# Optimization experiments

Hardware: AMD Instinct MI355X
Metric: run time of the kernel (lower is better)

The kernel has to match this reference:

```python
import jax, jax.numpy as jnp
import numpy as np

D_MODEL = 256; N_HEADS = 8; HEAD_DIM = 32; N_LEVELS = 4; N_POINTS = 4; N_LAYERS = 3; D_FFN = 1024
SHAPES = np.array([[76, 76], [38, 38], [19, 19], [10, 10]], dtype=np.int64)
S_TOTAL = int((SHAPES[:, 0] * SHAPES[:, 1]).sum())  # 7681


def setup_inputs():
    key = jax.random.key(0)
    ks = jax.random.split(key, 12)
    B = 1; C = D_MODEL; M = N_HEADS; Lv = N_LEVELS; P = N_POINTS; L = N_LAYERS; s = 0.02
    starts = np.concatenate([[0], np.cumsum(SHAPES[:, 0] * SHAPES[:, 1])[:-1]]).astype(np.int64)
    inp = {
        "src": jax.random.normal(ks[0], (B, S_TOTAL, C), jnp.float32),
        "pos": jax.random.normal(ks[1], (B, S_TOTAL, C), jnp.float32),
        "valid_ratios": jnp.ones((B, Lv, 2), jnp.float32),
        "spatial_shapes": jnp.asarray(SHAPES),
        "level_start_index": jnp.asarray(starts),
        "padding_mask": jnp.zeros((B, S_TOTAL), bool),
        "W_off": jax.random.normal(ks[2], (L, C, M * Lv * P * 2), jnp.float32) * s,
        "b_off": jax.random.normal(ks[3], (L, M * Lv * P * 2), jnp.float32) * s,
        "W_attn": jax.random.normal(ks[4], (L, C, M * Lv * P), jnp.float32) * s,
        "b_attn": jax.random.normal(ks[5], (L, M * Lv * P), jnp.float32) * s,
        "W_val": jax.random.normal(ks[6], (L, C, C), jnp.float32) * s,
        "b_val": jnp.zeros((L, C), jnp.float32),
        "W_out": jax.random.normal(ks[7], (L, C, C), jnp.float32) * s,
        "b_out": jnp.zeros((L, C), jnp.float32),
        "ln1_g": jnp.ones((L, C), jnp.float32),
        "ln1_b": jnp.zeros((L, C), jnp.float32),
        "W_ff1": jax.random.normal(ks[8], (L, C, D_FFN), jnp.float32) * s,
        "b_ff1": jnp.zeros((L, D_FFN), jnp.float32),
        "W_ff2": jax.random.normal(ks[9], (L, D_FFN, C), jnp.float32) * s,
        "b_ff2": jnp.zeros((L, C), jnp.float32),
        "ln2_g": jnp.ones((L, C), jnp.float32),
        "ln2_b": jnp.zeros((L, C), jnp.float32),
    }
    return inp


def _ln(x, g, b):
    mu = x.mean(-1, keepdims=True)
    var = ((x - mu) ** 2).mean(-1, keepdims=True)
    return (x - mu) * jax.lax.rsqrt(var + 1e-5) * g + b


def _gather(v, idx):
    # v: [B, HW, M, D], idx: [B, S, M, P] -> [B, S, M, P, D], head-specific gather
    B, S, M, P = idx.shape
    def one(vb, ib):
        i2 = ib.transpose(0, 2, 1).reshape(S * P, M, 1)
        o = jnp.take_along_axis(vb, i2, axis=0)  # [S*P, M, D]
        return o.reshape(S, P, M, -1).transpose(0, 2, 1, 3)
    return jax.vmap(one)(v, idx)


def _msda(query, src, mask, ref, shapes, starts, Wo, bo, Wa, ba, Wv, bv, Wout, bout):
    # Multi-scale deformable attention (Deformable-DETR), grid_sample align_corners=False + zero padding
    B, S, C = src.shape
    M, Lv, P, D = N_HEADS, N_LEVELS, N_POINTS, HEAD_DIM
    value = src @ Wv + bv
    value = jnp.where(mask[..., None], 0.0, value).reshape(B, S, M, D)
    off = (query @ Wo + bo).reshape(B, S, M, Lv, P, 2)
    aw = jax.nn.softmax((query @ Wa + ba).reshape(B, S, M, Lv * P), -1).reshape(B, S, M, Lv, P)
    norm = jnp.asarray(shapes[:, ::-1].copy(), jnp.float32)  # (W, H) per level
    loc = ref[:, :, None, :, None, :] + off / norm[None, None, None, :, None, :]  # [B,S,M,Lv,P,2]
    out = jnp.zeros((B, S, M, D), query.dtype)
    for lvl in range(Lv):
        H = int(shapes[lvl, 0]); W = int(shapes[lvl, 1]); st = int(starts[lvl])
        v = value[:, st:st + H * W]  # [B, H*W, M, D]
        l = loc[:, :, :, lvl]  # [B, S, M, P, 2]
        x = l[..., 0] * W - 0.5
        y = l[..., 1] * H - 0.5
        x0 = jnp.floor(x); y0 = jnp.floor(y)
        dx = x - x0; dy = y - y0
        samp = jnp.zeros((B, S, M, P, D), query.dtype)
        for yy, xx, w in ((y0, x0, (1 - dy) * (1 - dx)), (y0, x0 + 1, (1 - dy) * dx),
                          (y0 + 1, x0, dy * (1 - dx)), (y0 + 1, x0 + 1, dy * dx)):
            valid = (xx >= 0) & (xx < W) & (yy >= 0) & (yy < H)
            xi = jnp.clip(xx, 0, W - 1).astype(jnp.int32)
            yi = jnp.clip(yy, 0, H - 1).astype(jnp.int32)
            g = _gather(v, yi * W + xi)
            samp = samp + (w * valid)[..., None] * g
        out = out + (aw[:, :, :, lvl, :, None] * samp).sum(3)
    return out.reshape(B, S, C) @ Wout + bout


def _ref_points(vr, shapes):
    refs = []
    for lvl in range(shapes.shape[0]):
        H = int(shapes[lvl, 0]); W = int(shapes[lvl, 1])
        ry, rx = np.meshgrid(np.linspace(0.5, H - 0.5, H, dtype=np.float32),
                             np.linspace(0.5, W - 0.5, W, dtype=np.float32), indexing="ij")
        rxj = jnp.asarray(rx.reshape(-1))[None] / (vr[:, None, lvl, 0] * W)
        ryj = jnp.asarray(ry.reshape(-1))[None] / (vr[:, None, lvl, 1] * H)
        refs.append(jnp.stack([rxj, ryj], -1))
    ref = jnp.concatenate(refs, 1)  # [B, S, 2]
    return ref[:, :, None] * vr[:, None]  # [B, S, Lv, 2]


def _encoder(src, pos, valid_ratios, shapes, starts, mask, params):
    (W_off, b_off, W_attn, b_attn, W_val, b_val, W_out, b_out,
     ln1_g, ln1_b, W_ff1, b_ff1, W_ff2, b_ff2, ln2_g, ln2_b) = params
    ref = _ref_points(valid_ratios, shapes)
    out = src
    for l in range(N_LAYERS):
        q = out + pos  # with_pos_embed
        a = _msda(q, out, mask, ref, shapes, starts, W_off[l], b_off[l], W_attn[l], b_attn[l],
                  W_val[l], b_val[l], W_out[l], b_out[l])
        out = _ln(out + a, ln1_g[l], ln1_b[l])
        f = jax.nn.relu(out @ W_ff1[l] + b_ff1[l]) @ W_ff2[l] + b_ff2[l]
        out = _ln(out + f, ln2_g[l], ln2_b[l])
    return out


def reference(src, pos, valid_ratios, spatial_shapes, level_start_index, padding_mask,
              W_off, b_off, W_attn, b_attn, W_val, b_val, W_out, b_out,
              ln1_g, ln1_b, W_ff1, b_ff1, W_ff2, b_ff2, ln2_g, ln2_b):
    shapes = np.asarray(spatial_shapes)
    starts = np.asarray(level_start_index)
    params = (W_off, b_off, W_attn, b_attn, W_val, b_val, W_out, b_out,
              ln1_g, ln1_b, W_ff1, b_ff1, W_ff2, b_ff2, ln2_g, ln2_b)
    return _encoder(src, pos, valid_ratios, shapes, starts, padding_mask, params)
```

## Files before the change

### kernel.cpp

```cpp
#include <hip/hip_runtime.h>
#include <hip/hip_bf16.h>
#include <math.h>

#define S_TOTAL 7681

typedef __attribute__((ext_vector_type(8))) short bf16x8;
typedef __attribute__((ext_vector_type(4))) float f32x4;

__device__ __forceinline__ short f2b(float x) {
    union { float f; unsigned u; } v; v.f = x;
    unsigned r = v.u + 0x7FFFu + ((v.u >> 16) & 1u);
    return (short)(r >> 16);
}
__device__ __forceinline__ float b2f(unsigned short u) {
    union { unsigned u; float f; } t; t.u = ((unsigned)u) << 16; return t.f;
}

__global__ __launch_bounds__(256) void transpose_cvt_kernel(
    const float* __restrict__ s0, const float* __restrict__ s1,
    const float* __restrict__ s2, const float* __restrict__ s3,
    const float* __restrict__ s4, const float* __restrict__ s5,
    short* __restrict__ d0, short* __restrict__ d1, short* __restrict__ d2,
    short* __restrict__ d3, short* __restrict__ d4, short* __restrict__ d5)
{
    const int z = blockIdx.z;
    int t = blockIdx.x;
    const float* src; short* dst; int K, N, lt;
    if (t < 64)       { src = s0 + (size_t)z * 65536;  dst = d0 + (size_t)z * 65536;  K = 256;  N = 256;  lt = t; }
    else if (t < 128) { src = s1 + (size_t)z * 65536;  dst = d1 + (size_t)z * 98304;  K = 256;  N = 256;  lt = t - 64; }
    else if (t < 160) { src = s2 + (size_t)z * 32768;  dst = d2 + (size_t)z * 98304;  K = 256;  N = 128;  lt = t - 128; }
    else if (t < 224) { src = s3 + (size_t)z * 65536;  dst = d3 + (size_t)z * 65536;  K = 256;  N = 256;  lt = t - 160; }
    else if (t < 480) { src = s4 + (size_t)z * 262144; dst = d4 + (size_t)z * 262144; K = 256;  N = 1024; lt = t - 224; }
    else              { src = s5 + (size_t)z * 262144; dst = d5 + (size_t)z * 262144; K = 1024; N = 256;  lt = t - 480; }
    const int ntx = N >> 5;
    const int tk = (lt / ntx) << 5, tn = (lt % ntx) << 5;
    __shared__ float tile[32][33];
    const int cx = threadIdx.x & 31, cy = threadIdx.x >> 5;
    #pragma unroll
    for (int i = 0; i < 32; i += 8)
        tile[cy + i][cx] = src[(size_t)(tk + cy + i) * N + tn + cx];
    __syncthreads();
    #pragma unroll
    for (int i = 0; i < 32; i += 8)
        dst[(size_t)(tn + cy + i) * K + tk + cx] = f2b(tile[cx][cy + i]);
}

#define BM 128
#define BN 64
#define BK 32
#define KP 40

__global__ __launch_bounds__(256) void gemm_va_kernel(
    const short* __restrict__ xb, const short* __restrict__ qb,
    const short* __restrict__ Wt_val, const short* __restrict__ Wt_oa,
    const float* __restrict__ b_val, const float* __restrict__ b_off,
    const float* __restrict__ b_attn,
    short* __restrict__ value_bf, float* __restrict__ offbuf, int M)
{
    const int grp = (blockIdx.y >= 4);
    const short* A  = grp ? qb : xb;
    const short* Wt = grp ? Wt_oa : Wt_val;
    const int colBase = (grp ? (blockIdx.y - 4) : blockIdx.y) * BN;
    const int N = grp ? 384 : 256;
    const int K = 256;

    __shared__ __align__(16) short As[BM * KP];
    __shared__ __align__(16) short Bs[BN * KP];
    const int tid = threadIdx.x;
    const int lane = tid & 63;
    const int wave = tid >> 6;
    const int rowBase = blockIdx.x * BM;

    const int ar = tid >> 1;
    const int ak = (tid & 1) * 16;
    const int br = tid >> 2;
    const int bk = (tid & 3) * 8;

    const int frow = lane & 15;
    const int fko  = (lane >> 4) * 8;
    const int wm = wave * 32;

    f32x4 acc[2][4] = {};

    const int aRow = rowBase + ar;
    const bool aOk = aRow < M;
    const short* Ap = A + (size_t)aRow * K + ak;
    const short* Bp = Wt + (size_t)(colBase + br) * K + bk;

    bf16x8 a0 = {}, a1 = {}, b0 = {};
    if (aOk) { a0 = *(const bf16x8*)Ap; a1 = *(const bf16x8*)(Ap + 8); }
    b0 = *(const bf16x8*)Bp;

    for (int k0 = 0; k0 < K; k0 += BK) {
        *(bf16x8*)&As[ar * KP + ak]     = a0;
        *(bf16x8*)&As[ar * KP + ak + 8] = a1;
        *(bf16x8*)&Bs[br * KP + bk]     = b0;
        __syncthreads();

        const int kn = k0 + BK;
        if (kn < K) {
            if (aOk) { a0 = *(const bf16x8*)(Ap + kn); a1 = *(const bf16x8*)(Ap + kn + 8); }
            b0 = *(const bf16x8*)(Bp + kn);
        }

        bf16x8 af0 = *(const bf16x8*)&As[(wm + frow) * KP + fko];
        bf16x8 af1 = *(const bf16x8*)&As[(wm + 16 + frow) * KP + fko];
        #pragma unroll
        for (int j = 0; j < 4; ++j) {
            bf16x8 bfj = *(const bf16x8*)&Bs[(j * 16 + frow) * KP + fko];
            acc[0][j] = __builtin_amdgcn_mfma_f32_16x16x32_bf16(af0, bfj, acc[0][j], 0, 0, 0);
            acc[1][j] = __builtin_amdgcn_mfma_f32_16x16x32_bf16(af1, bfj, acc[1][j], 0, 0, 0);
        }
        __syncthreads();
    }

    const int erow = (lane >> 4) * 4;
    const int ecol = lane & 15;
    #pragma unroll
    for (int mi = 0; mi < 2; ++mi) {
        #pragma unroll
        for (int j = 0; j < 4; ++j) {
            int col = colBase + j * 16 + ecol;
            float bias = grp ? (col < 256 ? b_off[col] : b_attn[col - 256]) : b_val[col];
            #pragma unroll
            for (int r = 0; r < 4; ++r) {
                int row = rowBase + wm + mi * 16 + erow + r;
                if (row < M) {
                    float v = acc[mi][j][r] + bias;
                    if (grp) offbuf[(size_t)row * 384 + col] = v;
                    else     value_bf[(size_t)row * 256 + col] = f2b(v);
                }
            }
        }
    }
}

template<int RELU, int OUTBF>
__global__ __launch_bounds__(256) void gemm_kernel(
    const short* __restrict__ A, const short* __restrict__ Wt,
    const float* __restrict__ bias, void* __restrict__ Cv,
    int M, int N, int K)
{
    __shared__ __align__(16) short As[BM * KP];
    __shared__ __align__(16) short Bs[BN * KP];
    const int tid = threadIdx.x;
    const int lane = tid & 63;
    const int wave = tid >> 6;
    const int rowBase = blockIdx.x * BM;
    const int colBase = blockIdx.y * BN;

    const int ar = tid >> 1;
    const int ak = (tid & 1) * 16;
    const int br = tid >> 2;
    const int bk = (tid & 3) * 8;

    const int frow = lane & 15;
    const int fko  = (lane >> 4) * 8;
    const int wm = wave * 32;

    f32x4 acc[2][4] = {};

    const int aRow = rowBase + ar;
    const bool aOk = aRow < M;
    const short* Ap = A + (size_t)aRow * K + ak;
    const short* Bp = Wt + (size_t)(colBase + br) * K + bk;

    bf16x8 a0 = {}, a1 = {}, b0 = {};
    if (aOk) { a0 = *(const bf16x8*)Ap; a1 = *(const bf16x8*)(Ap + 8); }
    b0 = *(const bf16x8*)Bp;

    for (int k0 = 0; k0 < K; k0 += BK) {
        *(bf16x8*)&As[ar * KP + ak]     = a0;
        *(bf16x8*)&As[ar * KP + ak + 8] = a1;
        *(bf16x8*)&Bs[br * KP + bk]     = b0;
        __syncthreads();

        const int kn = k0 + BK;
        if (kn < K) {
            if (aOk) { a0 = *(const bf16x8*)(Ap + kn); a1 = *(const bf16x8*)(Ap + kn + 8); }
            b0 = *(const bf16x8*)(Bp + kn);
        }

        bf16x8 af0 = *(const bf16x8*)&As[(wm + frow) * KP + fko];
        bf16x8 af1 = *(const bf16x8*)&As[(wm + 16 + frow) * KP + fko];
        #pragma unroll
        for (int j = 0; j < 4; ++j) {
            bf16x8 bfj = *(const bf16x8*)&Bs[(j * 16 + frow) * KP + fko];
            acc[0][j] = __builtin_amdgcn_mfma_f32_16x16x32_bf16(af0, bfj, acc[0][j], 0, 0, 0);
            acc[1][j] = __builtin_amdgcn_mfma_f32_16x16x32_bf16(af1, bfj, acc[1][j], 0, 0, 0);
        }
        __syncthreads();
    }

    const int erow = (lane >> 4) * 4;
    const int ecol = lane & 15;
    #pragma unroll
    for (int mi = 0; mi < 2; ++mi) {
        #pragma unroll
        for (int j = 0; j < 4; ++j) {
            #pragma unroll
            for (int r = 0; r < 4; ++r) {
                int row = rowBase + wm + mi * 16 + erow + r;
                if (row < M) {
                    int col = colBase + j * 16 + ecol;
                    float v = acc[mi][j][r] + bias[col];
                    if (RELU) v = fmaxf(v, 0.f);
                    if (OUTBF) ((short*)Cv)[(size_t)row * N + col] = f2b(v);
                    else       ((float*)Cv)[(size_t)row * N + col] = v;
                }
            }
        }
    }
}

template<int WRITEQ>
__global__ __launch_bounds__(256) void gemm_ln_kernel(
    const short* __restrict__ A, const short* __restrict__ Wt,
    const float* __restrict__ bias, const float* __restrict__ g,
    const float* __restrict__ bln, const float* __restrict__ pos,
    float* __restrict__ out, short* __restrict__ xb, short* __restrict__ qb,
    int M, int K)
{
    __shared__ __align__(16) short As[32 * KP];
    __shared__ __align__(16) short Bs[256 * KP];
    __shared__ float rsum[32][4], rsq[32][4], smu[32], srs[32];

    const int tid = threadIdx.x;
    const int lane = tid & 63;
    const int wave = tid >> 6;
    const int rowBase = blockIdx.x * 32;

    const int frow = lane & 15;
    const int fko  = (lane >> 4) * 8;

    f32x4 acc[2][4] = {};

    const int ar = tid >> 1;
    const int ak = (tid & 1) * 16;
    const int aRow = rowBase + ar;
    const bool aOk = (tid < 64) && (aRow < M);
    const short* Ap = A + (size_t)aRow * K + ak;
    const short* Bp = Wt + (size_t)tid * K;

    bf16x8 a0 = {}, a1 = {};
    bf16x8 w0, w1, w2, w3;
    if (aOk) { a0 = *(const bf16x8*)Ap; a1 = *(const bf16x8*)(Ap + 8); }
    w0 = *(const bf16x8*)(Bp);      w1 = *(const bf16x8*)(Bp + 8);
    w2 = *(const bf16x8*)(Bp + 16); w3 = *(const bf16x8*)(Bp + 24);

    for (int k0 = 0; k0 < K; k0 += BK) {
        if (tid < 64) {
            *(bf16x8*)&As[ar * KP + ak]     = a0;
            *(bf16x8*)&As[ar * KP + ak + 8] = a1;
        }
        *(bf16x8*)&Bs[tid * KP + 0]  = w0;
        *(bf16x8*)&Bs[tid * KP + 8]  = w1;
        *(bf16x8*)&Bs[tid * KP + 16] = w2;
        *(bf16x8*)&Bs[tid * KP + 24] = w3;
        __syncthreads();

        const int kn = k0 + BK;
        if (kn < K) {
            if (aOk) { a0 = *(const bf16x8*)(Ap + kn); a1 = *(const bf16x8*)(Ap + kn + 8); }
            w0 = *(const bf16x8*)(Bp + kn);      w1 = *(const bf16x8*)(Bp + kn + 8);
            w2 = *(const bf16x8*)(Bp + kn + 16); w3 = *(const bf16x8*)(Bp + kn + 24);
        }

        bf16x8 af0 = *(const bf16x8*)&As[frow * KP + fko];
        bf16x8 af1 = *(const bf16x8*)&As[(16 + frow) * KP + fko];
        #pragma unroll
        for (int j = 0; j < 4; ++j) {
            bf16x8 bfj = *(const bf16x8*)&Bs[(wave * 64 + j * 16 + frow) * KP + fko];
            acc[0][j] = __builtin_amdgcn_mfma_f32_16x16x32_bf16(af0, bfj, acc[0][j], 0, 0, 0);
            acc[1][j] = __builtin_amdgcn_mfma_f32_16x16x32_bf16(af1, bfj, acc[1][j], 0, 0, 0);
        }
        __syncthreads();
    }

    const int erow = (lane >> 4) * 4;
    const int ecol = lane & 15;
    float x[2][4][4];
    #pragma unroll
    for (int mi = 0; mi < 2; ++mi)
        #pragma unroll
        for (int j = 0; j < 4; ++j)
            #pragma unroll
            for (int r = 0; r < 4; ++r) {
                int row = rowBase + mi * 16 + erow + r;
                int col = wave * 64 + j * 16 + ecol;
                float res = (row < M) ? out[(size_t)row * 256 + col] : 0.f;
                x[mi][j][r] = acc[mi][j][r] + bias[col] + res;
            }

    #pragma unroll
    for (int mi = 0; mi < 2; ++mi)
        #pragma unroll
        for (int r = 0; r < 4; ++r) {
            float s1 = x[mi][0][r] + x[mi][1][r] + x[mi][2][r] + x[mi][3][r];
            float s2 = x[mi][0][r]*x[mi][0][r] + x[mi][1][r]*x[mi][1][r]
                     + x[mi][2][r]*x[mi][2][r] + x[mi][3][r]*x[mi][3][r];
            #pragma unroll
            for (int o = 1; o < 16; o <<= 1) {
                s1 += __shfl_xor(s1, o);
                s2 += __shfl_xor(s2, o);
            }
            if ((lane & 15) == 0) {
                rsum[mi * 16 + erow + r][wave] = s1;
                rsq [mi * 16 + erow + r][wave] = s2;
            }
        }
    __syncthreads();
    if (tid < 32) {
        float S1 = rsum[tid][0] + rsum[tid][1] + rsum[tid][2] + rsum[tid][3];
        float S2 = rsq[tid][0] + rsq[tid][1] + rsq[tid][2] + rsq[tid][3];
        float mu = S1 * (1.f / 256.f);
        smu[tid] = mu;
        srs[tid] = rsqrtf(S2 * (1.f / 256.f) - mu * mu + 1e-5f);
    }
    __syncthreads();

    #pragma unroll
    for (int mi = 0; mi < 2; ++mi)
        #pragma unroll
        for (int r = 0; r < 4; ++r) {
            int lrow = mi * 16 + erow + r;
            int row = rowBase + lrow;
            if (row >= M) continue;
            float mu = smu[lrow], rs = srs[lrow];
            #pragma unroll
            for (int j = 0; j < 4; ++j) {
                int col = wave * 64 + j * 16 + ecol;
                float y = (x[mi][j][r] - mu) * rs * g[col] + bln[col];
                out[(size_t)row * 256 + col] = y;
                xb[(size_t)row * 256 + col] = f2b(y);
                if (WRITEQ)
                    qb[(size_t)row * 256 + col] = f2b(y + pos[(size_t)row * 256 + col]);
            }
        }
}

__global__ __launch_bounds__(256) void msda_kernel(
    const short* __restrict__ value, const float* __restrict__ offb,
    short* __restrict__ msdab)
{
    __shared__ float   soff[8 * 384];
    __shared__ ushort4 sIdx[1024];
    __shared__ float4  sWgt[1024];

    const int bid = blockIdx.x;
    const int sb = (bid & 7) * 121 + (bid >> 3);
    const int q0 = sb * 8;
    if (q0 >= S_TOTAL) return;
    const int tid = threadIdx.x;

    {
        const float4* src4 = (const float4*)offb;
        #pragma unroll
        for (int i = tid; i < 768; i += 256) {
            int qi = i / 96, j = i - qi * 96;
            int q = min(q0 + qi, S_TOTAL - 1);
            *(float4*)&soff[qi * 384 + j * 4] = src4[(size_t)q * 96 + j];
        }
    }
    __syncthreads();

    if (tid < 64) {
        const int qi = tid >> 3, m = tid & 7;
        float* lg = &soff[qi * 384 + 256 + m * 16];
        float mx = -1e30f;
        #pragma unroll
        for (int k = 0; k < 16; ++k) mx = fmaxf(mx, lg[k]);
        float e[16], sum = 0.f;
        #pragma unroll
        for (int k = 0; k < 16; ++k) { e[k] = expf(lg[k] - mx); sum += e[k]; }
        float inv = 1.f / sum;
        #pragma unroll
        for (int k = 0; k < 16; ++k) lg[k] = e[k] * inv;
    }
    __syncthreads();

    #pragma unroll
    for (int it = tid; it < 1024; it += 256) {
        const int qi = it >> 7, i = it & 127;
        const int lvl = (i >> 2) & 3;
        const int q = min(q0 + qi, S_TOTAL - 1);

        float refx, refy;
        if (q < 5776)      { int t = q;        int r = t / 76, c = t % 76; refx = (c + 0.5f) / 76.f; refy = (r + 0.5f) / 76.f; }
        else if (q < 7220) { int t = q - 5776; int r = t / 38, c = t % 38; refx = (c + 0.5f) / 38.f; refy = (r + 0.5f) / 38.f; }
        else if (q < 7581) { int t = q - 7220; int r = t / 19, c = t % 19; refx = (c + 0.5f) / 19.f; refy = (r + 0.5f) / 19.f; }
        else               { int t = q - 7581; int r = t / 10, c = t % 10; refx = (c + 0.5f) / 10.f; refy = (r + 0.5f) / 10.f; }

        const int LVL_HW[4] = {76, 38, 19, 10};
        const int LVL_ST[4] = {0, 5776, 7220, 7581};
        const int W = LVL_HW[lvl];
        const float fW = (float)W;

        float ox = soff[qi * 384 + i * 2];
        float oy = soff[qi * 384 + i * 2 + 1];
        float aw = soff[qi * 384 + 256 + i];

        float x = refx * fW + ox - 0.5f;
        float y = refy * fW + oy - 0.5f;
        float x0f = floorf(x), y0f = floorf(y);
        int x0 = (int)x0f, y0 = (int)y0f;
        float dx = x - x0f, dy = y - y0f;

        bool vx0 = (x0 >= 0) & (x0 < W);
        bool vx1 = (x0 >= -1) & (x0 < W - 1);
        bool vy0 = (y0 >= 0) & (y0 < W);
        bool vy1 = (y0 >= -1) & (y0 < W - 1);
        int xc0 = min(max(x0, 0), W - 1), xc1 = min(max(x0 + 1, 0), W - 1);
        int yc0 = min(max(y0, 0), W - 1), yc1 = min(max(y0 + 1, 0), W - 1);
        int base = LVL_ST[lvl];
        ushort4 id;
        id.x = (unsigned short)(base + yc0 * W + xc0);
        id.y = (unsigned short)(base + yc0 * W + xc1);
        id.z = (unsigned short)(base + yc1 * W + xc0);
        id.w = (unsigned short)(base + yc1 * W + xc1);
        float4 w4;
        w4.x = (vy0 && vx0) ? (1.f - dy) * (1.f - dx) * aw : 0.f;
        w4.y = (vy0 && vx1) ? (1.f - dy) * dx * aw : 0.f;
        w4.z = (vy1 && vx0) ? dy * (1.f - dx) * aw : 0.f;
        w4.w = (vy1 && vx1) ? dy * dx * aw : 0.f;
        sIdx[it] = id;
        sWgt[it] = w4;
    }
    __syncthreads();

    const int lane = tid & 63;
    const int qi = (tid >> 6) * 2 + (lane >> 5);
    const int q = q0 + qi;
    if (q >= S_TOTAL) return;
    const int l32 = lane & 31;
    const int h = l32 >> 2, dg = l32 & 3;
    const short* vcol = value + h * 32 + dg * 8;
    const int itb = qi * 128 + (h << 4);

    float a[8] = {};
    #pragma unroll
    for (int pt = 0; pt < 16; ++pt) {
        const ushort4 id = sIdx[itb + pt];
        const float4 w = sWgt[itb + pt];
        bf16x8 v0 = *(const bf16x8*)(vcol + ((size_t)id.x << 8));
        bf16x8 v1 = *(const bf16x8*)(vcol + ((size_t)id.y << 8));
        bf16x8 v2 = *(const bf16x8*)(vcol + ((size_t)id.z << 8));
        bf16x8 v3 = *(const bf16x8*)(vcol + ((size_t)id.w << 8));
        #pragma unroll
        for (int e = 0; e < 8; ++e)
            a[e] += w.x * b2f((unsigned short)v0[e]) + w.y * b2f((unsigned short)v1[e])
                  + w.z * b2f((unsigned short)v2[e]) + w.w * b2f((unsigned short)v3[e]);
    }
    bf16x8 o;
    #pragma unroll
    for (int e = 0; e < 8; ++e) o[e] = f2b(a[e]);
    *(bf16x8*)(msdab + (size_t)q * 256 + h * 32 + dg * 8) = o;
}

__global__ __launch_bounds__(256) void cvt_copy_kernel(
    const float4* __restrict__ src, const float4* __restrict__ pos,
    float4* __restrict__ o, ushort4* __restrict__ xb, ushort4* __restrict__ qb,
    int n4)
{
    int i = blockIdx.x * blockDim.x + threadIdx.x;
    if (i < n4) {
        float4 v = src[i], p = pos[i];
        o[i] = v;
        ushort4 h, hq;
        h.x = (unsigned short)f2b(v.x); h.y = (unsigned short)f2b(v.y);
        h.z = (unsigned short)f2b(v.z); h.w = (unsigned short)f2b(v.w);
        hq.x = (unsigned short)f2b(v.x + p.x); hq.y = (unsigned short)f2b(v.y + p.y);
        hq.z = (unsigned short)f2b(v.z + p.z); hq.w = (unsigned short)f2b(v.w + p.w);
        xb[i] = h;
        qb[i] = hq;
    }
}

extern "C" void kernel_launch(void* const* d_in, const int* in_sizes, int n_in,
                              void* d_out, int out_size, void* d_ws, size_t ws_size,
                              hipStream_t stream) {
    const float* src    = (const float*)d_in[0];
    const float* pos    = (const float*)d_in[1];
    const float* W_off  = (const float*)d_in[6];
    const float* b_off  = (const float*)d_in[7];
    const float* W_attn = (const float*)d_in[8];
    const float* b_attn = (const float*)d_in[9];
    const float* W_val  = (const float*)d_in[10];
    const float* b_val  = (const float*)d_in[11];
    const float* W_out  = (const float*)d_in[12];
    const float* b_out  = (const float*)d_in[13];
    const float* ln1_g  = (const float*)d_in[14];
    const float* ln1_b  = (const float*)d_in[15];
    const float* W_ff1  = (const float*)d_in[16];
    const float* b_ff1  = (const float*)d_in[17];
    const float* W_ff2  = (const float*)d_in[18];
    const float* b_ff2  = (const float*)d_in[19];
    const float* ln2_g  = (const float*)d_in[20];
    const float* ln2_b  = (const float*)d_in[21];

    const size_t S = S_TOTAL;
    float* out = (float*)d_out;

    short* wt = (short*)d_ws;
    short* Wt_val = wt;
    short* Wt_oa  = wt + 196608;
    short* Wt_out = wt + 491520;
    short* Wt_ff1 = wt + 688128;
    short* Wt_ff2 = wt + 1474560;
    float* fbase  = (float*)d_ws + 1131648;
    short* xb       = (short*)fbase;
    short* qb       = (short*)(fbase + 128 * S);
    short* value_bf = (short*)(fbase + 256 * S);
    float* offb     = fbase + 384 * S;
    short* msdab    = (short*)(fbase + 768 * S);
    short* hid      = (short*)(fbase + 256 * S);

    transpose_cvt_kernel<<<dim3(736, 1, 3), 256, 0, stream>>>(
        W_val, W_off, W_attn, W_out, W_ff1, W_ff2,
        Wt_val, Wt_oa, Wt_oa + 65536, Wt_out, Wt_ff1, Wt_ff2);

    const int n4 = (int)(S * 256 / 4);
    const int g4 = (n4 + 255) / 256;
    cvt_copy_kernel<<<g4, 256, 0, stream>>>((const float4*)src, (const float4*)pos,
                                            (float4*)out, (ushort4*)xb, (ushort4*)qb, n4);

    const int MB = (S_TOTAL + BM - 1) / BM;
    const int LB = (S_TOTAL + 31) / 32;

    for (int l = 0; l < 3; ++l) {
        gemm_va_kernel<<<dim3(MB, 10), 256, 0, stream>>>(
            xb, qb, Wt_val + (size_t)l * 65536, Wt_oa + (size_t)l * 98304,
            b_val + (size_t)l * 256, b_off + (size_t)l * 256, b_attn + (size_t)l * 128,
            value_bf, offb, S_TOTAL);
        msda_kernel<<<968, 256, 0, stream>>>(value_bf, offb, msdab);
        gemm_ln_kernel<0><<<LB, 256, 0, stream>>>(
            msdab, Wt_out + (size_t)l * 65536, b_out + (size_t)l * 256,
            ln1_g + (size_t)l * 256, ln1_b + (size_t)l * 256, pos,
            out, xb, qb, S_TOTAL, 256);
        gemm_kernel<1, 1><<<dim3(MB, 16), 256, 0, stream>>>(
            xb, Wt_ff1 + (size_t)l * 262144, b_ff1 + (size_t)l * 1024, hid,
            S_TOTAL, 1024, 256);
        gemm_ln_kernel<1><<<LB, 256, 0, stream>>>(
            hid, Wt_ff2 + (size_t)l * 262144, b_ff2 + (size_t)l * 256,
            ln2_g + (size_t)l * 256, ln2_b + (size_t)l * 256, pos,
            out, xb, qb, S_TOTAL, 1024);
    }
}
```

Baseline: 415.8 us.

## Fuse MSDA sampling into out-projection+LayerNorm and merge prologue kernels

The deformable-attention sampling kernel is fused with the output projection GEMM and LayerNorm. Each 16-row block samples its queries into shared memory and feeds them straight to MFMA, so the intermediate msda buffer no longer round-trips through global memory. The FF2+LN kernel now uses 16-row tiles, giving more blocks, and the weight transpose and input convert kernels are merged into one launch. In exchange, every 16-row block reloads the full out-projection and FF2 weights, and the fused kernel uses more shared memory, which may lower occupancy.

```diff
diff --git a/kernel.cpp b/kernel.cpp
--- a/kernel.cpp
+++ b/kernel.cpp
@@ -16,39 +16,58 @@
     union { unsigned u; float f; } t; t.u = ((unsigned)u) << 16; return t.f;
 }
 
-__global__ __launch_bounds__(256) void transpose_cvt_kernel(
+#define BM 128
+#define BN 64
+#define BK 32
+#define KP 40
+
+#define N4_TOT 491584
+__global__ __launch_bounds__(256) void prologue_kernel(
     const float* __restrict__ s0, const float* __restrict__ s1,
     const float* __restrict__ s2, const float* __restrict__ s3,
     const float* __restrict__ s4, const float* __restrict__ s5,
     short* __restrict__ d0, short* __restrict__ d1, short* __restrict__ d2,
-    short* __restrict__ d3, short* __restrict__ d4, short* __restrict__ d5)
+    short* __restrict__ d3, short* __restrict__ d4, short* __restrict__ d5,
+    const float4* __restrict__ src, const float4* __restrict__ pos,
+    float4* __restrict__ o, ushort4* __restrict__ xb, ushort4* __restrict__ qb)
 {
-    const int z = blockIdx.z;
-    int t = blockIdx.x;
-    const float* src; short* dst; int K, N, lt;
-    if (t < 64)       { src = s0 + (size_t)z * 65536;  dst = d0 + (size_t)z * 65536;  K = 256;  N = 256;  lt = t; }
-    else if (t < 128) { src = s1 + (size_t)z * 65536;  dst = d1 + (size_t)z * 98304;  K = 256;  N = 256;  lt = t - 64; }
-    else if (t < 160) { src = s2 + (size_t)z * 32768;  dst = d2 + (size_t)z * 98304;  K = 256;  N = 128;  lt = t - 128; }
-    else if (t < 224) { src = s3 + (size_t)z * 65536;  dst = d3 + (size_t)z * 65536;  K = 256;  N = 256;  lt = t - 160; }
-    else if (t < 480) { src = s4 + (size_t)z * 262144; dst = d4 + (size_t)z * 262144; K = 256;  N = 1024; lt = t - 224; }
-    else              { src = s5 + (size_t)z * 262144; dst = d5 + (size_t)z * 262144; K = 1024; N = 256;  lt = t - 480; }
+    int b = blockIdx.x;
+    if (b >= 2208) {
+        int i = (b - 2208) * 256 + threadIdx.x;
+        if (i < N4_TOT) {
+            float4 v = src[i], p = pos[i];
+            o[i] = v;
+            ushort4 h, hq;
+            h.x = (unsigned short)f2b(v.x); h.y = (unsigned short)f2b(v.y);
+            h.z = (unsigned short)f2b(v.z); h.w = (unsigned short)f2b(v.w);
+            hq.x = (unsigned short)f2b(v.x + p.x); hq.y = (unsigned short)f2b(v.y + p.y);
+            hq.z = (unsigned short)f2b(v.z + p.z); hq.w = (unsigned short)f2b(v.w + p.w);
+            xb[i] = h;
+            qb[i] = hq;
+        }
+        return;
+    }
+    const int z = b / 736;
+    int t = b - z * 736;
+    const float* src_w; short* dst; int K, N, lt;
+    if (t < 64)       { src_w = s0 + (size_t)z * 65536;  dst = d0 + (size_t)z * 65536;  K = 256;  N = 256;  lt = t; }
+    else if (t < 128) { src_w = s1 + (size_t)z * 65536;  dst = d1 + (size_t)z * 98304;  K = 256;  N = 256;  lt = t - 64; }
+    else if (t < 160) { src_w = s2 + (size_t)z * 32768;  dst = d2 + (size_t)z * 98304;  K = 256;  N = 128;  lt = t - 128; }
+    else if (t < 224) { src_w = s3 + (size_t)z * 65536;  dst = d3 + (size_t)z * 65536;  K = 256;  N = 256;  lt = t - 160; }
+    else if (t < 480) { src_w = s4 + (size_t)z * 262144; dst = d4 + (size_t)z * 262144; K = 256;  N = 1024; lt = t - 224; }
+    else              { src_w = s5 + (size_t)z * 262144; dst = d5 + (size_t)z * 262144; K = 1024; N = 256;  lt = t - 480; }
     const int ntx = N >> 5;
     const int tk = (lt / ntx) << 5, tn = (lt % ntx) << 5;
     __shared__ float tile[32][33];
     const int cx = threadIdx.x & 31, cy = threadIdx.x >> 5;
     #pragma unroll
     for (int i = 0; i < 32; i += 8)
-        tile[cy + i][cx] = src[(size_t)(tk + cy + i) * N + tn + cx];
+        tile[cy + i][cx] = src_w[(size_t)(tk + cy + i) * N + tn + cx];
     __syncthreads();
     #pragma unroll
     for (int i = 0; i < 32; i += 8)
         dst[(size_t)(tn + cy + i) * K + tk + cx] = f2b(tile[cx][cy + i]);
 }
-
-#define BM 128
-#define BN 64
-#define BK 32
-#define KP 40
 
 __global__ __launch_bounds__(256) void gemm_va_kernel(
     const short* __restrict__ xb, const short* __restrict__ qb,
@@ -61,7 +80,6 @@
     const short* A  = grp ? qb : xb;
     const short* Wt = grp ? Wt_oa : Wt_val;
     const int colBase = (grp ? (blockIdx.y - 4) : blockIdx.y) * BN;
-    const int N = grp ? 384 : 256;
     const int K = 256;
 
     __shared__ __align__(16) short As[BM * KP];
@@ -135,10 +153,9 @@
     }
 }
 
-template<int RELU, int OUTBF>
-__global__ __launch_bounds__(256) void gemm_kernel(
+__global__ __launch_bounds__(256) void gemm_ff1_kernel(
     const short* __restrict__ A, const short* __restrict__ Wt,
-    const float* __restrict__ bias, void* __restrict__ Cv,
+    const float* __restrict__ bias, short* __restrict__ Cv,
     int M, int N, int K)
 {
     __shared__ __align__(16) short As[BM * KP];
@@ -203,53 +220,261 @@
                 int row = rowBase + wm + mi * 16 + erow + r;
                 if (row < M) {
                     int col = colBase + j * 16 + ecol;
-                    float v = acc[mi][j][r] + bias[col];
-                    if (RELU) v = fmaxf(v, 0.f);
-                    if (OUTBF) ((short*)Cv)[(size_t)row * N + col] = f2b(v);
-                    else       ((float*)Cv)[(size_t)row * N + col] = v;
+                    float v = fmaxf(acc[mi][j][r] + bias[col], 0.f);
+                    Cv[(size_t)row * N + col] = f2b(v);
                 }
             }
         }
     }
 }
 
+__global__ __launch_bounds__(256) void msda_outln_kernel(
+    const short* __restrict__ value, const float* __restrict__ offb,
+    const short* __restrict__ Wt_out, const float* __restrict__ bias,
+    const float* __restrict__ g, const float* __restrict__ bln,
+    float* __restrict__ out, short* __restrict__ xb, int M)
+{
+    __shared__ __align__(16) char scratch[36864];
+    __shared__ __align__(16) short mt[16 * 264];
+    __shared__ float rsum[16][4], rsq[16][4], smu[16], srs[16];
+    float*   soff = (float*)scratch;
+    ushort4* sIdx = (ushort4*)(scratch + 12288);
+    float4*  sWgt = (float4*)(scratch + 20480);
+    short*   Bs   = (short*)scratch;
+
+    const int bid = blockIdx.x;
+    const int sb = (bid < 480) ? ((bid & 7) * 60 + (bid >> 3)) : 480;
+    const int q0 = sb * 16;
+    const int tid = threadIdx.x;
+    const int lane = tid & 63;
+    const int wave = tid >> 6;
+
+    for (int t = 0; t < 2; ++t) {
+        const int qs = q0 + t * 8;
+        {
+            const float4* src4 = (const float4*)offb;
+            float4* soff4 = (float4*)soff;
+            #pragma unroll
+            for (int i = tid; i < 768; i += 256) {
+                int qi = i / 96, j = i - qi * 96;
+                int q = min(qs + qi, S_TOTAL - 1);
+                soff4[qi * 96 + j] = src4[(size_t)q * 96 + j];
+            }
+        }
+        __syncthreads();
+
+        if (tid < 64) {
+            const int qi = tid >> 3, m = tid & 7;
+            float* lg = &soff[qi * 384 + 256 + m * 16];
+            float mx = -1e30f;
+            #pragma unroll
+            for (int k = 0; k < 16; ++k) mx = fmaxf(mx, lg[k]);
+            float e[16], sum = 0.f;
+            #pragma unroll
+            for (int k = 0; k < 16; ++k) { e[k] = expf(lg[k] - mx); sum += e[k]; }
+            float inv = 1.f / sum;
+            #pragma unroll
+            for (int k = 0; k < 16; ++k) lg[k] = e[k] * inv;
+        }
+        __syncthreads();
+
+        #pragma unroll
+        for (int it = tid; it < 1024; it += 256) {
+            const int qi = it >> 7, i = it & 127;
+            const int lvl = (i >> 2) & 3;
+            const int q = min(qs + qi, S_TOTAL - 1);
+
+            float refx, refy;
+            if (q < 5776)      { int u = q;        int r = u / 76, c = u % 76; refx = (c + 0.5f) / 76.f; refy = (r + 0.5f) / 76.f; }
+            else if (q < 7220) { int u = q - 5776; int r = u / 38, c = u % 38; refx = (c + 0.5f) / 38.f; refy = (r + 0.5f) / 38.f; }
+            else if (q < 7581) { int u = q - 7220; int r = u / 19, c = u % 19; refx = (c + 0.5f) / 19.f; refy = (r + 0.5f) / 19.f; }
+            else               { int u = q - 7581; int r = u / 10, c = u % 10; refx = (c + 0.5f) / 10.f; refy = (r + 0.5f) / 10.f; }
+
+            const int LVL_HW[4] = {76, 38, 19, 10};
+            const int LVL_ST[4] = {0, 5776, 7220, 7581};
+            const int W = LVL_HW[lvl];
+            const float fW = (float)W;
+
+            float ox = soff[qi * 384 + i * 2];
+            float oy = soff[qi * 384 + i * 2 + 1];
+            float aw = soff[qi * 384 + 256 + i];
+
+            float x = refx * fW + ox - 0.5f;
+            float y = refy * fW + oy - 0.5f;
+            float x0f = floorf(x), y0f = floorf(y);
+            int x0 = (int)x0f, y0 = (int)y0f;
+            float dx = x - x0f, dy = y - y0f;
+
+            bool vx0 = (x0 >= 0) & (x0 < W);
+            bool vx1 = (x0 >= -1) & (x0 < W - 1);
+            bool vy0 = (y0 >= 0) & (y0 < W);
+            bool vy1 = (y0 >= -1) & (y0 < W - 1);
+            int xc0 = min(max(x0, 0), W - 1), xc1 = min(max(x0 + 1, 0), W - 1);
+            int yc0 = min(max(y0, 0), W - 1), yc1 = min(max(y0 + 1, 0), W - 1);
+            int base = LVL_ST[lvl];
+            ushort4 id;
+            id.x = (unsigned short)(base + yc0 * W + xc0);
+            id.y = (unsigned short)(base + yc0 * W + xc1);
+            id.z = (unsigned short)(base + yc1 * W + xc0);
+            id.w = (unsigned short)(base + yc1 * W + xc1);
+            float4 w4;
+            w4.x = (vy0 && vx0) ? (1.f - dy) * (1.f - dx) * aw : 0.f;
+            w4.y = (vy0 && vx1) ? (1.f - dy) * dx * aw : 0.f;
+            w4.z = (vy1 && vx0) ? dy * (1.f - dx) * aw : 0.f;
+            w4.w = (vy1 && vx1) ? dy * dx * aw : 0.f;
+            sIdx[it] = id;
+            sWgt[it] = w4;
+        }
+        __syncthreads();
+
+        {
+            const int qi = wave * 2 + ((lane >> 5) & 1);
+            const int l32 = lane & 31;
+            const int h = l32 >> 2, dg = l32 & 3;
+            const short* vcol = value + h * 32 + dg * 8;
+            const int itb = qi * 128 + (h << 4);
+
+            float a[8] = {};
+            #pragma unroll
+            for (int pt = 0; pt < 16; ++pt) {
+                const ushort4 id = sIdx[itb + pt];
+                const float4 w = sWgt[itb + pt];
+                bf16x8 v0 = *(const bf16x8*)(vcol + ((size_t)id.x << 8));
+                bf16x8 v1 = *(const bf16x8*)(vcol + ((size_t)id.y << 8));
+                bf16x8 v2 = *(const bf16x8*)(vcol + ((size_t)id.z << 8));
+                bf16x8 v3 = *(const bf16x8*)(vcol + ((size_t)id.w << 8));
+                #pragma unroll
+                for (int e = 0; e < 8; ++e)
+                    a[e] += w.x * b2f((unsigned short)v0[e]) + w.y * b2f((unsigned short)v1[e])
+                          + w.z * b2f((unsigned short)v2[e]) + w.w * b2f((unsigned short)v3[e]);
+            }
+            bf16x8 o;
+            #pragma unroll
+            for (int e = 0; e < 8; ++e) o[e] = f2b(a[e]);
+            *(bf16x8*)&mt[(t * 8 + qi) * 264 + h * 32 + dg * 8] = o;
+        }
+        __syncthreads();
+    }
+
+    const int frow = lane & 15;
+    const int fko  = (lane >> 4) * 8;
+
+    f32x4 acc[4] = {};
+    const short* Bp = Wt_out + (size_t)tid * 256;
+    bf16x8 w0 = *(const bf16x8*)(Bp);      bf16x8 w1 = *(const bf16x8*)(Bp + 8);
+    bf16x8 w2 = *(const bf16x8*)(Bp + 16); bf16x8 w3 = *(const bf16x8*)(Bp + 24);
+
+    for (int k0 = 0; k0 < 256; k0 += BK) {
+        *(bf16x8*)&Bs[tid * KP + 0]  = w0;
+        *(bf16x8*)&Bs[tid * KP + 8]  = w1;
+        *(bf16x8*)&Bs[tid * KP + 16] = w2;
+        *(bf16x8*)&Bs[tid * KP + 24] = w3;
+        __syncthreads();
+
+        const int kn = k0 + BK;
+        if (kn < 256) {
+            w0 = *(const bf16x8*)(Bp + kn);      w1 = *(const bf16x8*)(Bp + kn + 8);
+            w2 = *(const bf16x8*)(Bp + kn + 16); w3 = *(const bf16x8*)(Bp + kn + 24);
+        }
+
+        bf16x8 af = *(const bf16x8*)&mt[frow * 264 + k0 + fko];
+        #pragma unroll
+        for (int j = 0; j < 4; ++j) {
+            bf16x8 bfj = *(const bf16x8*)&Bs[(wave * 64 + j * 16 + frow) * KP + fko];
+            acc[j] = __builtin_amdgcn_mfma_f32_16x16x32_bf16(af, bfj, acc[j], 0, 0, 0);
+        }
+        __syncthreads();
+    }
+
+    const int erow = (lane >> 4) * 4;
+    const int ecol = lane & 15;
+    float x[4][4];
+    #pragma unroll
+    for (int j = 0; j < 4; ++j)
+        #pragma unroll
+        for (int r = 0; r < 4; ++r) {
+            int row = q0 + erow + r;
+            int col = wave * 64 + j * 16 + ecol;
+            float res = (row < M) ? out[(size_t)row * 256 + col] : 0.f;
+            x[j][r] = acc[j][r] + bias[col] + res;
+        }
+
+    #pragma unroll
+    for (int r = 0; r < 4; ++r) {
+        float s1 = x[0][r] + x[1][r] + x[2][r] + x[3][r];
+        float s2 = x[0][r]*x[0][r] + x[1][r]*x[1][r] + x[2][r]*x[2][r] + x[3][r]*x[3][r];
+        #pragma unroll
+        for (int o = 1; o < 16; o <<= 1) {
+            s1 += __shfl_xor(s1, o);
+            s2 += __shfl_xor(s2, o);
+        }
+        if ((lane & 15) == 0) {
+            rsum[erow + r][wave] = s1;
+            rsq [erow + r][wave] = s2;
+        }
+    }
+    __syncthreads();
+    if (tid < 16) {
+        float S1 = rsum[tid][0] + rsum[tid][1] + rsum[tid][2] + rsum[tid][3];
+        float S2 = rsq[tid][0] + rsq[tid][1] + rsq[tid][2] + rsq[tid][3];
+        float mu = S1 * (1.f / 256.f);
+        smu[tid] = mu;
+        srs[tid] = rsqrtf(S2 * (1.f / 256.f) - mu * mu + 1e-5f);
+    }
+    __syncthreads();
+
+    #pragma unroll
+    for (int r = 0; r < 4; ++r) {
+        int lrow = erow + r;
+        int row = q0 + lrow;
+        if (row >= M) continue;
+        float mu = smu[lrow], rs = srs[lrow];
+        #pragma unroll
+        for (int j = 0; j < 4; ++j) {
+            int col = wave * 64 + j * 16 + ecol;
+            float y = (x[j][r] - mu) * rs * g[col] + bln[col];
+            out[(size_t)row * 256 + col] = y;
+            xb[(size_t)row * 256 + col] = f2b(y);
+        }
+    }
+}
+
 template<int WRITEQ>
-__global__ __launch_bounds__(256) void gemm_ln_kernel(
+__global__ __launch_bounds__(256) void gemm_ln16_kernel(
     const short* __restrict__ A, const short* __restrict__ Wt,
     const float* __restrict__ bias, const float* __restrict__ g,
     const float* __restrict__ bln, const float* __restrict__ pos,
     float* __restrict__ out, short* __restrict__ xb, short* __restrict__ qb,
     int M, int K)
 {
-    __shared__ __align__(16) short As[32 * KP];
+    __shared__ __align__(16) short As[16 * KP];
     __shared__ __align__(16) short Bs[256 * KP];
-    __shared__ float rsum[32][4], rsq[32][4], smu[32], srs[32];
+    __shared__ float rsum[16][4], rsq[16][4], smu[16], srs[16];
 
     const int tid = threadIdx.x;
     const int lane = tid & 63;
     const int wave = tid >> 6;
-    const int rowBase = blockIdx.x * 32;
+    const int rowBase = blockIdx.x * 16;
 
     const int frow = lane & 15;
     const int fko  = (lane >> 4) * 8;
 
-    f32x4 acc[2][4] = {};
+    f32x4 acc[4] = {};
 
     const int ar = tid >> 1;
     const int ak = (tid & 1) * 16;
     const int aRow = rowBase + ar;
-    const bool aOk = (tid < 64) && (aRow < M);
+    const bool aOk = (tid < 32) && (aRow < M);
     const short* Ap = A + (size_t)aRow * K + ak;
     const short* Bp = Wt + (size_t)tid * K;
 
     bf16x8 a0 = {}, a1 = {};
-    bf16x8 w0, w1, w2, w3;
     if (aOk) { a0 = *(const bf16x8*)Ap; a1 = *(const bf16x8*)(Ap + 8); }
-    w0 = *(const bf16x8*)(Bp);      w1 = *(const bf16x8*)(Bp + 8);
-    w2 = *(const bf16x8*)(Bp + 16); w3 = *(const bf16x8*)(Bp + 24);
+    bf16x8 w0 = *(const bf16x8*)(Bp);      bf16x8 w1 = *(const bf16x8*)(Bp + 8);
+    bf16x8 w2 = *(const bf16x8*)(Bp + 16); bf16x8 w3 = *(const bf16x8*)(Bp + 24);
 
     for (int k0 = 0; k0 < K; k0 += BK) {
-        if (tid < 64) {
+        if (tid < 32) {
             *(bf16x8*)&As[ar * KP + ak]     = a0;
             *(bf16x8*)&As[ar * KP + ak + 8] = a1;
         }
@@ -266,51 +491,44 @@
             w2 = *(const bf16x8*)(Bp + kn + 16); w3 = *(const bf16x8*)(Bp + kn + 24);
         }
 
-        bf16x8 af0 = *(const bf16x8*)&As[frow * KP + fko];
-        bf16x8 af1 = *(const bf16x8*)&As[(16 + frow) * KP + fko];
+        bf16x8 af = *(const bf16x8*)&As[frow * KP + fko];
         #pragma unroll
         for (int j = 0; j < 4; ++j) {
             bf16x8 bfj = *(const bf16x8*)&Bs[(wave * 64 + j * 16 + frow) * KP + fko];
-            acc[0][j] = __builtin_amdgcn_mfma_f32_16x16x32_bf16(af0, bfj, acc[0][j], 0, 0, 0);
-            acc[1][j] = __builtin_amdgcn_mfma_f32_16x16x32_bf16(af1, bfj, acc[1][j], 0, 0, 0);
+            acc[j] = __builtin_amdgcn_mfma_f32_16x16x32_bf16(af, bfj, acc[j], 0, 0, 0);
         }
         __syncthreads();
     }
 
     const int erow = (lane >> 4) * 4;
     const int ecol = lane & 15;
-    float x[2][4][4];
-    #pragma unroll
-    for (int mi = 0; mi < 2; ++mi)
-        #pragma unroll
-        for (int j = 0; j < 4; ++j)
-            #pragma unroll
-            for (int r = 0; r < 4; ++r) {
-                int row = rowBase + mi * 16 + erow + r;
-                int col = wave * 64 + j * 16 + ecol;
-                float res = (row < M) ? out[(size_t)row * 256 + col] : 0.f;
-                x[mi][j][r] = acc[mi][j][r] + bias[col] + res;
-            }
-
-    #pragma unroll
-    for (int mi = 0; mi < 2; ++mi)
+    float x[4][4];
+    #pragma unroll
+    for (int j = 0; j < 4; ++j)
         #pragma unroll
         for (int r = 0; r < 4; ++r) {
-            float s1 = x[mi][0][r] + x[mi][1][r] + x[mi][2][r] + x[mi][3][r];
-            float s2 = x[mi][0][r]*x[mi][0][r] + x[mi][1][r]*x[mi][1][r]
-                     + x[mi][2][r]*x[mi][2][r] + x[mi][3][r]*x[mi][3][r];
-            #pragma unroll
-            for (int o = 1; o < 16; o <<= 1) {
-                s1 += __shfl_xor(s1, o);
-                s2 += __shfl_xor(s2, o);
-            }
-            if ((lane & 15) == 0) {
-                rsum[mi * 16 + erow + r][wave] = s1;
-                rsq [mi * 16 + erow + r][wave] = s2;
-            }
-        }
+            int row = rowBase + erow + r;
+            int col = wave * 64 + j * 16 + ecol;
+            float res = (row < M) ? out[(size_t)row * 256 + col] : 0.f;
+            x[j][r] = acc[j][r] + bias[col] + res;
+        }
+
+    #pragma unroll
+    for (int r = 0; r < 4; ++r) {
+        float s1 = x[0][r] + x[1][r] + x[2][r] + x[3][r];
+        float s2 = x[0][r]*x[0][r] + x[1][r]*x[1][r] + x[2][r]*x[2][r] + x[3][r]*x[3][r];
+        #pragma unroll
+        for (int o = 1; o < 16; o <<= 1) {
+            s1 += __shfl_xor(s1, o);
+            s2 += __shfl_xor(s2, o);
+        }
+        if ((lane & 15) == 0) {
+            rsum[erow + r][wave] = s1;
+            rsq [erow + r][wave] = s2;
+        }
+    }
     __syncthreads();
-    if (tid < 32) {
+    if (tid < 16) {
         float S1 = rsum[tid][0] + rsum[tid][1] + rsum[tid][2] + rsum[tid][3];
         float S2 = rsq[tid][0] + rsq[tid][1] + rsq[tid][2] + rsq[tid][3];
         float mu = S1 * (1.f / 256.f);
@@ -320,159 +538,20 @@
     __syncthreads();
 
     #pragma unroll
-    for (int mi = 0; mi < 2; ++mi)
-        #pragma unroll
-        for (int r = 0; r < 4; ++r) {
-            int lrow = mi * 16 + erow + r;
-            int row = rowBase + lrow;
-            if (row >= M) continue;
-            float mu = smu[lrow], rs = srs[lrow];
-            #pragma unroll
-            for (int j = 0; j < 4; ++j) {
-                int col = wave * 64 + j * 16 + ecol;
-                float y = (x[mi][j][r] - mu) * rs * g[col] + bln[col];
-                out[(size_t)row * 256 + col] = y;
-                xb[(size_t)row * 256 + col] = f2b(y);
-                if (WRITEQ)
-                    qb[(size_t)row * 256 + col] = f2b(y + pos[(size_t)row * 256 + col]);
-            }
-        }
-}
-
-__global__ __launch_bounds__(256) void msda_kernel(
-    const short* __restrict__ value, const float* __restrict__ offb,
-    short* __restrict__ msdab)
-{
-    __shared__ float   soff[8 * 384];
-    __shared__ ushort4 sIdx[1024];
-    __shared__ float4  sWgt[1024];
-
-    const int bid = blockIdx.x;
-    const int sb = (bid & 7) * 121 + (bid >> 3);
-    const int q0 = sb * 8;
-    if (q0 >= S_TOTAL) return;
-    const int tid = threadIdx.x;
-
-    {
-        const float4* src4 = (const float4*)offb;
-        #pragma unroll
-        for (int i = tid; i < 768; i += 256) {
-            int qi = i / 96, j = i - qi * 96;
-            int q = min(q0 + qi, S_TOTAL - 1);
-            *(float4*)&soff[qi * 384 + j * 4] = src4[(size_t)q * 96 + j];
-        }
-    }
-    __syncthreads();
-
-    if (tid < 64) {
-        const int qi = tid >> 3, m = tid & 7;
-        float* lg = &soff[qi * 384 + 256 + m * 16];
-        float mx = -1e30f;
-        #pragma unroll
-        for (int k = 0; k < 16; ++k) mx = fmaxf(mx, lg[k]);
-        float e[16], sum = 0.f;
-        #pragma unroll
-        for (int k = 0; k < 16; ++k) { e[k] = expf(lg[k] - mx); sum += e[k]; }
-        float inv = 1.f / sum;
-        #pragma unroll
-        for (int k = 0; k < 16; ++k) lg[k] = e[k] * inv;
-    }
-    __syncthreads();
-
-    #pragma unroll
-    for (int it = tid; it < 1024; it += 256) {
-        const int qi = it >> 7, i = it & 127;
-        const int lvl = (i >> 2) & 3;
-        const int q = min(q0 + qi, S_TOTAL - 1);
-
-        float refx, refy;
-        if (q < 5776)      { int t = q;        int r = t / 76, c = t % 76; refx = (c + 0.5f) / 76.f; refy = (r + 0.5f) / 76.f; }
-        else if (q < 7220) { int t = q - 5776; int r = t / 38, c = t % 38; refx = (c + 0.5f) / 38.f; refy = (r + 0.5f) / 38.f; }
-        else if (q < 7581) { int t = q - 7220; int r = t / 19, c = t % 19; refx = (c + 0.5f) / 19.f; refy = (r + 0.5f) / 19.f; }
-        else               { int t = q - 7581; int r = t / 10, c = t % 10; refx = (c + 0.5f) / 10.f; refy = (r + 0.5f) / 10.f; }
-
-        const int LVL_HW[4] = {76, 38, 19, 10};
-        const int LVL_ST[4] = {0, 5776, 7220, 7581};
-        const int W = LVL_HW[lvl];
-        const float fW = (float)W;
-
-        float ox = soff[qi * 384 + i * 2];
-        float oy = soff[qi * 384 + i * 2 + 1];
-        float aw = soff[qi * 384 + 256 + i];
-
-        float x = refx * fW + ox - 0.5f;
-        float y = refy * fW + oy - 0.5f;
-        float x0f = floorf(x), y0f = floorf(y);
-        int x0 = (int)x0f, y0 = (int)y0f;
-        float dx = x - x0f, dy = y - y0f;
-
-        bool vx0 = (x0 >= 0) & (x0 < W);
-        bool vx1 = (x0 >= -1) & (x0 < W - 1);
-        bool vy0 = (y0 >= 0) & (y0 < W);
-        bool vy1 = (y0 >= -1) & (y0 < W - 1);
-        int xc0 = min(max(x0, 0), W - 1), xc1 = min(max(x0 + 1, 0), W - 1);
-        int yc0 = min(max(y0, 0), W - 1), yc1 = min(max(y0 + 1, 0), W - 1);
-        int base = LVL_ST[lvl];
-        ushort4 id;
-        id.x = (unsigned short)(base + yc0 * W + xc0);
-        id.y = (unsigned short)(base + yc0 * W + xc1);
-        id.z = (unsigned short)(base + yc1 * W + xc0);
-        id.w = (unsigned short)(base + yc1 * W + xc1);
-        float4 w4;
-        w4.x = (vy0 && vx0) ? (1.f - dy) * (1.f - dx) * aw : 0.f;
-        w4.y = (vy0 && vx1) ? (1.f - dy) * dx * aw : 0.f;
-        w4.z = (vy1 && vx0) ? dy * (1.f - dx) * aw : 0.f;
-        w4.w = (vy1 && vx1) ? dy * dx * aw : 0.f;
-        sIdx[it] = id;
-        sWgt[it] = w4;
-    }
-    __syncthreads();
-
-    const int lane = tid & 63;
-    const int qi = (tid >> 6) * 2 + (lane >> 5);
-    const int q = q0 + qi;
-    if (q >= S_TOTAL) return;
-    const int l32 = lane & 31;
-    const int h = l32 >> 2, dg = l32 & 3;
-    const short* vcol = value + h * 32 + dg * 8;
-    const int itb = qi * 128 + (h << 4);
-
-    float a[8] = {};
-    #pragma unroll
-    for (int pt = 0; pt < 16; ++pt) {
-        const ushort4 id = sIdx[itb + pt];
-        const float4 w = sWgt[itb + pt];
-        bf16x8 v0 = *(const bf16x8*)(vcol + ((size_t)id.x << 8));
-        bf16x8 v1 = *(const bf16x8*)(vcol + ((size_t)id.y << 8));
-        bf16x8 v2 = *(const bf16x8*)(vcol + ((size_t)id.z << 8));
-        bf16x8 v3 = *(const bf16x8*)(vcol + ((size_t)id.w << 8));
-        #pragma unroll
-        for (int e = 0; e < 8; ++e)
-            a[e] += w.x * b2f((unsigned short)v0[e]) + w.y * b2f((unsigned short)v1[e])
-                  + w.z * b2f((unsigned short)v2[e]) + w.w * b2f((unsigned short)v3[e]);
-    }
-    bf16x8 o;
-    #pragma unroll
-    for (int e = 0; e < 8; ++e) o[e] = f2b(a[e]);
-    *(bf16x8*)(msdab + (size_t)q * 256 + h * 32 + dg * 8) = o;
-}
-
-__global__ __launch_bounds__(256) void cvt_copy_kernel(
-    const float4* __restrict__ src, const float4* __restrict__ pos,
-    float4* __restrict__ o, ushort4* __restrict__ xb, ushort4* __restrict__ qb,
-    int n4)
-{
-    int i = blockIdx.x * blockDim.x + threadIdx.x;
-    if (i < n4) {
-        float4 v = src[i], p = pos[i];
-        o[i] = v;
-        ushort4 h, hq;
-        h.x = (unsigned short)f2b(v.x); h.y = (unsigned short)f2b(v.y);
-        h.z = (unsigned short)f2b(v.z); h.w = (unsigned short)f2b(v.w);
-        hq.x = (unsigned short)f2b(v.x + p.x); hq.y = (unsigned short)f2b(v.y + p.y);
-        hq.z = (unsigned short)f2b(v.z + p.z); hq.w = (unsigned short)f2b(v.w + p.w);
-        xb[i] = h;
-        qb[i] = hq;
+    for (int r = 0; r < 4; ++r) {
+        int lrow = erow + r;
+        int row = rowBase + lrow;
+        if (row >= M) continue;
+        float mu = smu[lrow], rs = srs[lrow];
+        #pragma unroll
+        for (int j = 0; j < 4; ++j) {
+            int col = wave * 64 + j * 16 + ecol;
+            float y = (x[j][r] - mu) * rs * g[col] + bln[col];
+            out[(size_t)row * 256 + col] = y;
+            xb[(size_t)row * 256 + col] = f2b(y);
+            if (WRITEQ)
+                qb[(size_t)row * 256 + col] = f2b(y + pos[(size_t)row * 256 + col]);
+        }
     }
 }
 
@@ -512,35 +591,30 @@
     short* qb       = (short*)(fbase + 128 * S);
     short* value_bf = (short*)(fbase + 256 * S);
     float* offb     = fbase + 384 * S;
-    short* msdab    = (short*)(fbase + 768 * S);
     short* hid      = (short*)(fbase + 256 * S);
 
-    transpose_cvt_kernel<<<dim3(736, 1, 3), 256, 0, stream>>>(
+    prologue_kernel<<<4129, 256, 0, stream>>>(
         W_val, W_off, W_attn, W_out, W_ff1, W_ff2,
-        Wt_val, Wt_oa, Wt_oa + 65536, Wt_out, Wt_ff1, Wt_ff2);
-
-    const int n4 = (int)(S * 256 / 4);
-    const int g4 = (n4 + 255) / 256;
-    cvt_copy_kernel<<<g4, 256, 0, stream>>>((const float4*)src, (const float4*)pos,
-                                            (float4*)out, (ushort4*)xb, (ushort4*)qb, n4);
+        Wt_val, Wt_oa, Wt_oa + 65536, Wt_out, Wt_ff1, Wt_ff2,
+        (const float4*)src, (const float4*)pos,
+        (float4*)out, (ushort4*)xb, (ushort4*)qb);
 
     const int MB = (S_TOTAL + BM - 1) / BM;
-    const int LB = (S_TOTAL + 31) / 32;
+    const int LB = (S_TOTAL + 15) / 16;
 
     for (int l = 0; l < 3; ++l) {
         gemm_va_kernel<<<dim3(MB, 10), 256, 0, stream>>>(
             xb, qb, Wt_val + (size_t)l * 65536, Wt_oa + (size_t)l * 98304,
             b_val + (size_t)l * 256, b_off + (size_t)l * 256, b_attn + (size_t)l * 128,
             value_bf, offb, S_TOTAL);
-        msda_kernel<<<968, 256, 0, stream>>>(value_bf, offb, msdab);
-        gemm_ln_kernel<0><<<LB, 256, 0, stream>>>(
-            msdab, Wt_out + (size_t)l * 65536, b_out + (size_t)l * 256,
-            ln1_g + (size_t)l * 256, ln1_b + (size_t)l * 256, pos,
-            out, xb, qb, S_TOTAL, 256);
-        gemm_kernel<1, 1><<<dim3(MB, 16), 256, 0, stream>>>(
+        msda_outln_kernel<<<LB, 256, 0, stream>>>(
+            value_bf, offb, Wt_out + (size_t)l * 65536, b_out + (size_t)l * 256,
+            ln1_g + (size_t)l * 256, ln1_b + (size_t)l * 256,
+            out, xb, S_TOTAL);
+        gemm_ff1_kernel<<<dim3(MB, 16), 256, 0, stream>>>(
             xb, Wt_ff1 + (size_t)l * 262144, b_ff1 + (size_t)l * 1024, hid,
             S_TOTAL, 1024, 256);
-        gemm_ln_kernel<1><<<LB, 256, 0, stream>>>(
+        gemm_ln16_kernel<1><<<LB, 256, 0, stream>>>(
             hid, Wt_ff2 + (size_t)l * 262144, b_ff2 + (size_t)l * 256,
             ln2_g + (size_t)l * 256, ln2_b + (size_t)l * 256, pos,
             out, xb, qb, S_TOTAL, 1024);
```

Result: slower. 449.1 us (+8.0%).
